# Kernel optimization log

Hardware: AMD Instinct MI355X
Metric: run time of the kernel (lower is better)

The kernel has to match this reference:

```python
import jax, jax.numpy as jnp
import numpy as np

BATCH, SEQ, IN, HID = 128, 512, 128, 1024

def setup_inputs() -> dict:
    key = jax.random.key(0)
    ks = jax.random.split(key, 7)
    s = 0.02  # small init so tanh/sigmoid stay in useful range
    return {
        "x": jax.random.normal(ks[0], (BATCH, SEQ, IN), dtype=jnp.float32),
        "W0": jax.random.normal(ks[1], (IN + HID, 3 * HID), dtype=jnp.float32) * s,
        "b0": jnp.zeros((3 * HID,), dtype=jnp.float32),
        "W1": jax.random.normal(ks[2], (HID + HID, 3 * HID), dtype=jnp.float32) * s,
        "b1": jnp.zeros((3 * HID,), dtype=jnp.float32),
        "Wfc": jax.random.normal(ks[3], (HID, 1), dtype=jnp.float32) * s,
        "bfc": jnp.zeros((1,), dtype=jnp.float32),
    }

def reference(x, W0, b0, W1, b1, Wfc, bfc):
    # Faithful to the torch module: note reset_gate/combined_reset are computed
    # but NEVER used for new_gate in the original -- new_gate = tanh(gates chunk 3)
    # from the [input, h_prev] projection. We reproduce that exact math.
    batch = x.shape[0]
    Ws, bs = (W0, W1), (b0, b1)
    h0 = tuple(jnp.zeros((batch, HID), dtype=x.dtype) for _ in range(2))

    def step(hs, x_t):
        inp = x_t
        new_hs = []
        for W, b, h in zip(Ws, bs, hs):
            gates = jnp.concatenate([inp, h], axis=1) @ W + b  # (B, 3H)
            z, _r, n = jnp.split(gates, 3, axis=1)
            z = jax.nn.sigmoid(z)
            n = jnp.tanh(n)
            h = (1.0 - z) * n + z * h
            new_hs.append(h)
            inp = h
        return tuple(new_hs), inp  # inp == last layer h_next

    x_t = jnp.transpose(x, (1, 0, 2))  # (S, B, IN)
    _, outs = jax.lax.scan(step, h0, x_t)  # outs: (S, B, H)
    # predictions[:, -1, :].squeeze(): only the final timestep matters
    pred_last = outs[-1] @ Wfc + bfc  # (B, 1)
    return jnp.squeeze(pred_last, axis=-1)  # (B,)
```

## Files before the change

### kernel.cpp

```cpp
#include <hip/hip_runtime.h>
#include <hip/hip_bf16.h>
#include <stdint.h>


#define SEQLEN 512
#define INDIM  128

typedef short bhalf8 __attribute__((ext_vector_type(8)));
typedef float f32x4  __attribute__((ext_vector_type(4)));

#define WS_H0B 4096
#define WS_H1B (WS_H0B + 2*262144)
#define WS_H1F (WS_H1B + 2*262144)
#define WS_END (WS_H1F + 524288)
#define LDS_BYTES 163840

__device__ __forceinline__ unsigned int bfbits(float f) {
  __hip_bfloat16 h = __float2bfloat16(f);
  unsigned short u; __builtin_memcpy(&u, &h, 2);
  return (unsigned int)u;
}

template<int N> __device__ __forceinline__ void waitvm() {
  asm volatile("s_waitcnt vmcnt(%0)" :: "n"(N));
}

#define GLOADA(dst, p)  asm volatile("global_load_dwordx4 %0, %1, off sc0 sc1" : "=v"(dst) : "v"((unsigned long long)(p)))
#define STORE_BF16(p, u) asm volatile("global_store_short %0, %1, off sc0 sc1" :: "v"((unsigned long long)(p)), "v"(u))
#define STORE_F32(p, f)  asm volatile("global_store_dword %0, %1, off sc0 sc1" :: "v"((unsigned long long)(p)), "v"(f))

#define ATIE(sI) asm volatile("" : "+v"(af[sI][0]), "+v"(af[sI][1]), "+v"(af[sI][2]), "+v"(af[sI][3]))

#define MFMA4(ntI, bx, sI) \
  acc[0][ntI] = __builtin_amdgcn_mfma_f32_16x16x32_bf16(af[sI][0], bx, acc[0][ntI], 0,0,0); \
  acc[1][ntI] = __builtin_amdgcn_mfma_f32_16x16x32_bf16(af[sI][1], bx, acc[1][ntI], 0,0,0); \
  acc[2][ntI] = __builtin_amdgcn_mfma_f32_16x16x32_bf16(af[sI][2], bx, acc[2][ntI], 0,0,0); \
  acc[3][ntI] = __builtin_amdgcn_mfma_f32_16x16x32_bf16(af[sI][3], bx, acc[3][ntI], 0,0,0);

#define MFMA4X(ntI, bx) \
  acc[0][ntI] = __builtin_amdgcn_mfma_f32_16x16x32_bf16(ax[0], bx, acc[0][ntI], 0,0,0); \
  acc[1][ntI] = __builtin_amdgcn_mfma_f32_16x16x32_bf16(ax[1], bx, acc[1][ntI], 0,0,0); \
  acc[2][ntI] = __builtin_amdgcn_mfma_f32_16x16x32_bf16(ax[2], bx, acc[2][ntI], 0,0,0); \
  acc[3][ntI] = __builtin_amdgcn_mfma_f32_16x16x32_bf16(ax[3], bx, acc[3][ntI], 0,0,0);

#define LDSB0(ntI, kb) (*(const bhalf8*)(smem + ((ntI)*16 + l15)*2304 + ((kb) ^ swz)))
#define LDSB1(ntI, kb) (*(const bhalf8*)(smem + ((ntI)*16 + l15)*4096 + ((kb) ^ swz)))

#define L0H(i) { \
  waitvm<((i) <= 4 ? 12 : 4*(7-(i)))>(); \
  ATIE((i)&3); \
  { const int kb = 256 + ks*512 + (i)*64 + l4*16; \
    bhalf8 bv0 = LDSB0(0, kb); bhalf8 bv1 = LDSB0(1, kb); \
    bhalf8 bv2 = LDSB0(2, kb); bhalf8 bv3 = LDSB0(3, kb); \
    MFMA4(0, bv0, (i)&3); MFMA4(1, bv1, (i)&3); \
    MFMA4(2, bv2, (i)&3); MFMA4(3, bv3, (i)&3); } \
  if ((i) + 4 < 8) { \
    GLOADA(af[(i)&3][0], abase0 + ((i)+4)*32); \
    GLOADA(af[(i)&3][1], abase1 + ((i)+4)*32); \
    GLOADA(af[(i)&3][2], abase2 + ((i)+4)*32); \
    GLOADA(af[(i)&3][3], abase3 + ((i)+4)*32); } \
}

#define L1H(i) { \
  waitvm<((i) <= 12 ? 12 : 4*(15-(i)))>(); \
  ATIE((i)&3); \
  { const int kb = ks*1024 + (i)*64 + l4*16; \
    bhalf8 bv0 = LDSB1(0, kb); bhalf8 bv1 = LDSB1(1, kb); \
    MFMA4(0, bv0, (i)&3); MFMA4(1, bv1, (i)&3); } \
  if ((i) + 4 < 16) { \
    GLOADA(af[(i)&3][0], abase0 + ((i)+4)*32); \
    GLOADA(af[(i)&3][1], abase1 + ((i)+4)*32); \
    GLOADA(af[(i)&3][2], abase2 + ((i)+4)*32); \
    GLOADA(af[(i)&3][3], abase3 + ((i)+4)*32); } \
}

__global__ __launch_bounds__(256, 1) void gru_persist(
    const float* __restrict__ x,  const float* __restrict__ W0,
    const float* __restrict__ b0, const float* __restrict__ W1,
    const float* __restrict__ b1, char* __restrict__ ws)
{
  extern __shared__ char smem[];
  const int tid  = threadIdx.x;
  const int lane = tid & 63;
  const int ks   = tid >> 6;
  const int l4   = lane >> 4;
  const int l15  = lane & 15;
  const int swz  = (l15 & 7) << 4;
  const int wg   = blockIdx.x;
  const bool isL0 = wg < 64;

  unsigned short* h0b = (unsigned short*)(ws + WS_H0B);
  unsigned short* h1b = (unsigned short*)(ws + WS_H1B);
  float*          h1f = (float*)(ws + WS_H1F);
  unsigned int*   bar = (unsigned int*)ws;

  int g, blk;
  if (isL0) { g = wg & 1; blk = wg >> 1; }
  else      { int idx = wg - 64; g = idx & 1; blk = idx >> 1; }

  if (isL0) {
    const int n   = lane;
    const int col = (n < 32) ? (blk*32 + n) : (2048 + blk*32 + (n - 32));
    for (int it = 0; it < 288; ++it) {
      const int k = ks*288 + it;
      unsigned int u = bfbits(W0[(size_t)k*3072 + col]);
      *(unsigned short*)(smem + n*2304 + ((2*k) ^ ((n & 7) << 4))) = (unsigned short)u;
    }
  } else {
    const int n   = lane & 31;
    const int col = (n < 16) ? (blk*16 + n) : (2048 + blk*16 + (n - 16));
    for (int it = 0; it < 256; ++it) {
      const int k = ks*512 + it*2 + (lane >> 5);
      unsigned int u = bfbits(W1[(size_t)k*3072 + col]);
      *(unsigned short*)(smem + n*4096 + ((2*k) ^ ((n & 7) << 4))) = (unsigned short)u;
    }
  }
  __syncthreads();

  float biasv[4] = {0.f, 0.f, 0.f, 0.f};
  if (isL0) {
    biasv[0] = b0[blk*32 + l15];
    biasv[1] = b0[blk*32 + 16 + l15];
    biasv[2] = b0[2048 + blk*32 + l15];
    biasv[3] = b0[2048 + blk*32 + 16 + l15];
  } else {
    biasv[0] = b1[blk*16 + l15];
    biasv[1] = b1[2048 + blk*16 + l15];
  }

  float hp[2][4] = {{0.f,0.f,0.f,0.f},{0.f,0.f,0.f,0.f}};

  for (int p = 0; p <= SEQLEN; ++p) {
    if (isL0) {
      if (p < SEQLEN) {
        const int t = p;
        const unsigned short* h0in  = h0b + (size_t)((t+1)&1)*131072;
        unsigned short*       h0out = h0b + (size_t)(t&1)*131072;

        f32x4 acc[4][4];
        #pragma unroll
        for (int mt = 0; mt < 4; ++mt)
          #pragma unroll
          for (int nt = 0; nt < 4; ++nt)
            #pragma unroll
            for (int r = 0; r < 4; ++r)
              acc[mt][nt][r] = (ks == 0) ? biasv[nt] : 0.0f;

        {
          bhalf8 ax[4];
          #pragma unroll
          for (int mt = 0; mt < 4; ++mt) {
            const int b = g*64 + mt*16 + l15;
            const float* xp = x + ((size_t)b*SEQLEN + t)*INDIM + ks*32 + l4*8;
            f32x4 lo = *(const f32x4*)xp;
            f32x4 hi = *(const f32x4*)(xp + 4);
            #pragma unroll
            for (int e = 0; e < 4; ++e) {
              ax[mt][e]   = (short)bfbits(lo[e]);
              ax[mt][4+e] = (short)bfbits(hi[e]);
            }
          }
          const int kb = ks*64 + l4*16;
          bhalf8 bv0 = LDSB0(0, kb); bhalf8 bv1 = LDSB0(1, kb);
          bhalf8 bv2 = LDSB0(2, kb); bhalf8 bv3 = LDSB0(3, kb);
          MFMA4X(0, bv0); MFMA4X(1, bv1); MFMA4X(2, bv2); MFMA4X(3, bv3);
        }

        const int bb = g*64 + l15;
        const unsigned short* abase0 = h0in + (size_t)(bb +  0)*1024 + ks*256 + l4*8;
        const unsigned short* abase1 = h0in + (size_t)(bb + 16)*1024 + ks*256 + l4*8;
        const unsigned short* abase2 = h0in + (size_t)(bb + 32)*1024 + ks*256 + l4*8;
        const unsigned short* abase3 = h0in + (size_t)(bb + 48)*1024 + ks*256 + l4*8;
        bhalf8 af[4][4];
        GLOADA(af[0][0], abase0 +  0); GLOADA(af[0][1], abase1 +  0);
        GLOADA(af[0][2], abase2 +  0); GLOADA(af[0][3], abase3 +  0);
        GLOADA(af[1][0], abase0 + 32); GLOADA(af[1][1], abase1 + 32);
        GLOADA(af[1][2], abase2 + 32); GLOADA(af[1][3], abase3 + 32);
        GLOADA(af[2][0], abase0 + 64); GLOADA(af[2][1], abase1 + 64);
        GLOADA(af[2][2], abase2 + 64); GLOADA(af[2][3], abase3 + 64);
        GLOADA(af[3][0], abase0 + 96); GLOADA(af[3][1], abase1 + 96);
        GLOADA(af[3][2], abase2 + 96); GLOADA(af[3][3], abase3 + 96);
        L0H(0) L0H(1) L0H(2) L0H(3) L0H(4) L0H(5) L0H(6) L0H(7)

        float* st = (float*)(smem + 147456);
        f32x4 gacc[4];
        #pragma unroll
        for (int q = 0; q < 4; ++q) {
          __syncthreads();
          #pragma unroll
          for (int nt = 0; nt < 4; ++nt)
            #pragma unroll
            for (int r = 0; r < 4; ++r)
              st[ks*1024 + nt*256 + (l4*4+r)*16 + l15] = acc[q][nt][r];
          __syncthreads();
          if (ks == q) {
            #pragma unroll
            for (int nt = 0; nt < 4; ++nt)
              #pragma unroll
              for (int r = 0; r < 4; ++r)
                gacc[nt][r] = st[       nt*256 + (l4*4+r)*16 + l15]
                            + st[1024 + nt*256 + (l4*4+r)*16 + l15]
                            + st[2048 + nt*256 + (l4*4+r)*16 + l15]
                            + st[3072 + nt*256 + (l4*4+r)*16 + l15];
          }
        }

        #pragma unroll
        for (int pi = 0; pi < 2; ++pi)
          #pragma unroll
          for (int r = 0; r < 4; ++r) {
            const float z  = 1.0f/(1.0f + __expf(-gacc[pi][r]));
            const float e2 = __expf(2.0f*gacc[pi+2][r]);
            const float n  = (e2 - 1.0f)/(e2 + 1.0f);
            const float hn = n + z*(hp[pi][r] - n);
            hp[pi][r] = hn;
            const int j = blk*32 + pi*16 + l15;
            const int b = g*64 + ks*16 + l4*4 + r;
            STORE_BF16(h0out + (size_t)b*1024 + j, bfbits(hn));
          }
      }
    } else {
      if (p > 0) {
        const int t = p - 1;
        const unsigned short* h0in  = h0b + (size_t)(t&1)*131072;
        const unsigned short* h1in  = h1b + (size_t)((t+1)&1)*131072;
        unsigned short*       h1out = h1b + (size_t)(t&1)*131072;

        f32x4 acc[4][2];
        #pragma unroll
        for (int mt = 0; mt < 4; ++mt)
          #pragma unroll
          for (int nt = 0; nt < 2; ++nt)
            #pragma unroll
            for (int r = 0; r < 4; ++r)
              acc[mt][nt][r] = (ks == 0) ? biasv[nt] : 0.0f;

        const unsigned short* asrc = (ks < 2) ? h0in : h1in;
        const int bb = g*64 + l15;
        const unsigned short* abase0 = asrc + (size_t)(bb +  0)*1024 + (ks&1)*512 + l4*8;
        const unsigned short* abase1 = asrc + (size_t)(bb + 16)*1024 + (ks&1)*512 + l4*8;
        const unsigned short* abase2 = asrc + (size_t)(bb + 32)*1024 + (ks&1)*512 + l4*8;
        const unsigned short* abase3 = asrc + (size_t)(bb + 48)*1024 + (ks&1)*512 + l4*8;
        bhalf8 af[4][4];
        GLOADA(af[0][0], abase0 +  0); GLOADA(af[0][1], abase1 +  0);
        GLOADA(af[0][2], abase2 +  0); GLOADA(af[0][3], abase3 +  0);
        GLOADA(af[1][0], abase0 + 32); GLOADA(af[1][1], abase1 + 32);
        GLOADA(af[1][2], abase2 + 32); GLOADA(af[1][3], abase3 + 32);
        GLOADA(af[2][0], abase0 + 64); GLOADA(af[2][1], abase1 + 64);
        GLOADA(af[2][2], abase2 + 64); GLOADA(af[2][3], abase3 + 64);
        GLOADA(af[3][0], abase0 + 96); GLOADA(af[3][1], abase1 + 96);
        GLOADA(af[3][2], abase2 + 96); GLOADA(af[3][3], abase3 + 96);
        L1H(0)  L1H(1)  L1H(2)  L1H(3)  L1H(4)  L1H(5)  L1H(6)  L1H(7)
        L1H(8)  L1H(9)  L1H(10) L1H(11) L1H(12) L1H(13) L1H(14) L1H(15)

        float* st = (float*)(smem + 131072);
        f32x4 gacc[2];
        #pragma unroll
        for (int q = 0; q < 4; ++q) {
          __syncthreads();
          #pragma unroll
          for (int nt = 0; nt < 2; ++nt)
            #pragma unroll
            for (int r = 0; r < 4; ++r)
              st[ks*512 + nt*256 + (l4*4+r)*16 + l15] = acc[q][nt][r];
          __syncthreads();
          if (ks == q) {
            #pragma unroll
            for (int nt = 0; nt < 2; ++nt)
              #pragma unroll
              for (int r = 0; r < 4; ++r)
                gacc[nt][r] = st[       nt*256 + (l4*4+r)*16 + l15]
                            + st[ 512 + nt*256 + (l4*4+r)*16 + l15]
                            + st[1024 + nt*256 + (l4*4+r)*16 + l15]
                            + st[1536 + nt*256 + (l4*4+r)*16 + l15];
          }
        }

        #pragma unroll
        for (int r = 0; r < 4; ++r) {
          const float z  = 1.0f/(1.0f + __expf(-gacc[0][r]));
          const float e2 = __expf(2.0f*gacc[1][r]);
          const float n  = (e2 - 1.0f)/(e2 + 1.0f);
          const float hn = n + z*(hp[0][r] - n);
          hp[0][r] = hn;
          const int j = blk*16 + l15;
          const int b = g*64 + ks*16 + l4*4 + r;
          STORE_BF16(h1out + (size_t)b*1024 + j, bfbits(hn));
          STORE_F32(h1f + (size_t)b*1024 + j, hn);
        }
      }
    }

    asm volatile("s_waitcnt vmcnt(0) lgkmcnt(0)" ::: "memory");
    __syncthreads();
    if (tid == 0) {
      __hip_atomic_fetch_add(&bar[(wg & 7)*32], 1u, __ATOMIC_RELAXED, __HIP_MEMORY_SCOPE_AGENT);
      const unsigned int target = 24u * (unsigned int)(p + 1);
      for (;;) {
        unsigned int mn = 0xffffffffu;
        #pragma unroll
        for (int c = 0; c < 8; ++c) {
          unsigned int v = __hip_atomic_load(&bar[c*32], __ATOMIC_RELAXED, __HIP_MEMORY_SCOPE_AGENT);
          mn = (v < mn) ? v : mn;
        }
        if (mn >= target) break;
        __builtin_amdgcn_s_sleep(1);
      }
    }
    __syncthreads();
  }
}

__global__ void gru_pred(const char* __restrict__ ws, const float* __restrict__ Wfc,
                         const float* __restrict__ bfc, float* __restrict__ out)
{
  const int b = blockIdx.x;
  const int l = threadIdx.x;
  const float* h = (const float*)(ws + WS_H1F) + (size_t)b*1024;
  float s = 0.0f;
  for (int k = l; k < 1024; k += 64) s += h[k] * Wfc[k];
  #pragma unroll
  for (int off = 32; off > 0; off >>= 1) s += __shfl_down(s, off);
  if (l == 0) out[b] = s + bfc[0];
}

extern "C" void kernel_launch(void* const* d_in, const int* in_sizes, int n_in,
                              void* d_out, int out_size, void* d_ws, size_t ws_size,
                              hipStream_t stream)
{
  (void)in_sizes; (void)n_in; (void)out_size; (void)ws_size;
  const float* x   = (const float*)d_in[0];
  const float* W0  = (const float*)d_in[1];
  const float* b0  = (const float*)d_in[2];
  const float* W1  = (const float*)d_in[3];
  const float* b1  = (const float*)d_in[4];
  const float* Wfc = (const float*)d_in[5];
  const float* bfc = (const float*)d_in[6];
  char* ws = (char*)d_ws;

  hipFuncSetAttribute(reinterpret_cast<const void*>(gru_persist),
                      hipFuncAttributeMaxDynamicSharedMemorySize, LDS_BYTES);
  hipMemsetAsync(ws, 0, WS_END, stream);
  hipLaunchKernelGGL(gru_persist, dim3(192), dim3(256), LDS_BYTES, stream,
                     x, W0, b0, W1, b1, ws);
  hipLaunchKernelGGL(gru_pred, dim3(128), dim3(64), 0, stream,
                     ws, Wfc, bfc, (float*)d_out);
}
```

Baseline: 5.835 ms.

## Replace global grid barrier with per-row-block dataflow flags and full-K waves

Replaces the per-timestep grid-wide atomic barrier with fine-grained per-row-block, per-column-group progress flags, so each wave waits only on the producers it actually reads. Each wave now covers the full K dimension for its own batch rows, which removes the cross-wave LDS split-K reduction and its __syncthreads. Hidden-state buffers are quadruple-buffered so layer 0 can run up to three steps ahead of layer 1. The layer-1 fp32 state is written only at the last step. The cost is more global loads per wave and many flag polls, and correctness now depends on the release fence and flag ordering.

New measurement: 13.78 ms. 136% more time.

```diff
diff --git a/kernel.cpp b/kernel.cpp
--- a/kernel.cpp
+++ b/kernel.cpp
@@ -4,310 +4,265 @@
 
 
 #define SEQLEN 512
-#define INDIM  128
 
 typedef short bhalf8 __attribute__((ext_vector_type(8)));
 typedef float f32x4  __attribute__((ext_vector_type(4)));
 
-#define WS_H0B 4096
-#define WS_H1B (WS_H0B + 2*262144)
-#define WS_H1F (WS_H1B + 2*262144)
-#define WS_END (WS_H1F + 524288)
-#define LDS_BYTES 163840
+#define OFF_F0   0
+#define OFF_F1   2048
+#define OFF_H0   8192
+#define OFF_H1   (OFF_H0 + 4*262144)
+#define OFF_H1F  (OFF_H1 + 4*262144)
+#define WS_END   (OFF_H1F + 524288)
+#define LDS_BYTES 131072
 
 __device__ __forceinline__ unsigned int bfbits(float f) {
   __hip_bfloat16 h = __float2bfloat16(f);
   unsigned short u; __builtin_memcpy(&u, &h, 2);
   return (unsigned int)u;
 }
-
 template<int N> __device__ __forceinline__ void waitvm() {
   asm volatile("s_waitcnt vmcnt(%0)" :: "n"(N));
 }
-
-#define GLOADA(dst, p)  asm volatile("global_load_dwordx4 %0, %1, off sc0 sc1" : "=v"(dst) : "v"((unsigned long long)(p)))
-#define STORE_BF16(p, u) asm volatile("global_store_short %0, %1, off sc0 sc1" :: "v"((unsigned long long)(p)), "v"(u))
-#define STORE_F32(p, f)  asm volatile("global_store_dword %0, %1, off sc0 sc1" :: "v"((unsigned long long)(p)), "v"(f))
-
-#define ATIE(sI) asm volatile("" : "+v"(af[sI][0]), "+v"(af[sI][1]), "+v"(af[sI][2]), "+v"(af[sI][3]))
-
-#define MFMA4(ntI, bx, sI) \
-  acc[0][ntI] = __builtin_amdgcn_mfma_f32_16x16x32_bf16(af[sI][0], bx, acc[0][ntI], 0,0,0); \
-  acc[1][ntI] = __builtin_amdgcn_mfma_f32_16x16x32_bf16(af[sI][1], bx, acc[1][ntI], 0,0,0); \
-  acc[2][ntI] = __builtin_amdgcn_mfma_f32_16x16x32_bf16(af[sI][2], bx, acc[2][ntI], 0,0,0); \
-  acc[3][ntI] = __builtin_amdgcn_mfma_f32_16x16x32_bf16(af[sI][3], bx, acc[3][ntI], 0,0,0);
-
-#define MFMA4X(ntI, bx) \
-  acc[0][ntI] = __builtin_amdgcn_mfma_f32_16x16x32_bf16(ax[0], bx, acc[0][ntI], 0,0,0); \
-  acc[1][ntI] = __builtin_amdgcn_mfma_f32_16x16x32_bf16(ax[1], bx, acc[1][ntI], 0,0,0); \
-  acc[2][ntI] = __builtin_amdgcn_mfma_f32_16x16x32_bf16(ax[2], bx, acc[2][ntI], 0,0,0); \
-  acc[3][ntI] = __builtin_amdgcn_mfma_f32_16x16x32_bf16(ax[3], bx, acc[3][ntI], 0,0,0);
-
-#define LDSB0(ntI, kb) (*(const bhalf8*)(smem + ((ntI)*16 + l15)*2304 + ((kb) ^ swz)))
-#define LDSB1(ntI, kb) (*(const bhalf8*)(smem + ((ntI)*16 + l15)*4096 + ((kb) ^ swz)))
-
-#define L0H(i) { \
-  waitvm<((i) <= 4 ? 12 : 4*(7-(i)))>(); \
-  ATIE((i)&3); \
-  { const int kb = 256 + ks*512 + (i)*64 + l4*16; \
-    bhalf8 bv0 = LDSB0(0, kb); bhalf8 bv1 = LDSB0(1, kb); \
-    bhalf8 bv2 = LDSB0(2, kb); bhalf8 bv3 = LDSB0(3, kb); \
-    MFMA4(0, bv0, (i)&3); MFMA4(1, bv1, (i)&3); \
-    MFMA4(2, bv2, (i)&3); MFMA4(3, bv3, (i)&3); } \
-  if ((i) + 4 < 8) { \
-    GLOADA(af[(i)&3][0], abase0 + ((i)+4)*32); \
-    GLOADA(af[(i)&3][1], abase1 + ((i)+4)*32); \
-    GLOADA(af[(i)&3][2], abase2 + ((i)+4)*32); \
-    GLOADA(af[(i)&3][3], abase3 + ((i)+4)*32); } \
-}
-
-#define L1H(i) { \
-  waitvm<((i) <= 12 ? 12 : 4*(15-(i)))>(); \
-  ATIE((i)&3); \
-  { const int kb = ks*1024 + (i)*64 + l4*16; \
-    bhalf8 bv0 = LDSB1(0, kb); bhalf8 bv1 = LDSB1(1, kb); \
-    MFMA4(0, bv0, (i)&3); MFMA4(1, bv1, (i)&3); } \
-  if ((i) + 4 < 16) { \
-    GLOADA(af[(i)&3][0], abase0 + ((i)+4)*32); \
-    GLOADA(af[(i)&3][1], abase1 + ((i)+4)*32); \
-    GLOADA(af[(i)&3][2], abase2 + ((i)+4)*32); \
-    GLOADA(af[(i)&3][3], abase3 + ((i)+4)*32); } \
-}
-
-__global__ __launch_bounds__(256, 1) void gru_persist(
+#define GLOADA(dst, p)  asm volatile("global_load_dwordx4 %0, %1, off sc0 sc1" : "=v"(dst) : "v"((unsigned long long)(p)) : "memory")
+#define STORE_BF16(p,u) asm volatile("global_store_short %0, %1, off sc0 sc1" :: "v"((unsigned long long)(p)), "v"(u) : "memory")
+#define STORE_F32(p,f)  asm volatile("global_store_dword %0, %1, off sc0 sc1" :: "v"((unsigned long long)(p)), "v"(f) : "memory")
+#define RELEASE_FENCE() __builtin_amdgcn_fence(__ATOMIC_RELEASE, "agent")
+
+#define MFMA(a,b,c) __builtin_amdgcn_mfma_f32_16x16x32_bf16((a),(b),(c),0,0,0)
+
+#define L0I(i) { \
+  waitvm<((i) < 28 ? 6 : 2*(31-(i)))>(); \
+  asm volatile("" : "+v"(af[(i)&3][0]), "+v"(af[(i)&3][1])); \
+  { const int kb = 256 + (i)*64 + l4*16; \
+    bhalf8 bvz = *(const bhalf8*)(smem + l15*2304 + (kb ^ swz)); \
+    bhalf8 bvn = *(const bhalf8*)(smem + (16+l15)*2304 + (kb ^ swz)); \
+    acc[0][0] = MFMA(af[(i)&3][0], bvz, acc[0][0]); \
+    acc[0][1] = MFMA(af[(i)&3][0], bvn, acc[0][1]); \
+    acc[1][0] = MFMA(af[(i)&3][1], bvz, acc[1][0]); \
+    acc[1][1] = MFMA(af[(i)&3][1], bvn, acc[1][1]); } \
+  if ((i)+4 < 32) { GLOADA(af[(i)&3][0], ab0 + ((i)+4)*32); \
+                    GLOADA(af[(i)&3][1], ab1 + ((i)+4)*32); } \
+}
+
+#define L1I(i, KOFF, abx) { \
+  waitvm<((i) < 24 ? 7 : (31-(i)))>(); \
+  asm volatile("" : "+v"(af[(i)&7])); \
+  { const int kb = (KOFF) + (i)*64 + l4*16; \
+    bhalf8 bvz = *(const bhalf8*)(smem + l15*4096 + (kb ^ swz)); \
+    bhalf8 bvn = *(const bhalf8*)(smem + (16+l15)*4096 + (kb ^ swz)); \
+    accz = MFMA(af[(i)&7], bvz, accz); \
+    accn = MFMA(af[(i)&7], bvn, accn); } \
+  if ((i)+8 < 32) { GLOADA(af[(i)&7], (abx) + ((i)+8)*32); } \
+}
+
+#define L1HALF(KOFF, abx) \
+  L1I(0,KOFF,abx)  L1I(1,KOFF,abx)  L1I(2,KOFF,abx)  L1I(3,KOFF,abx)  \
+  L1I(4,KOFF,abx)  L1I(5,KOFF,abx)  L1I(6,KOFF,abx)  L1I(7,KOFF,abx)  \
+  L1I(8,KOFF,abx)  L1I(9,KOFF,abx)  L1I(10,KOFF,abx) L1I(11,KOFF,abx) \
+  L1I(12,KOFF,abx) L1I(13,KOFF,abx) L1I(14,KOFF,abx) L1I(15,KOFF,abx) \
+  L1I(16,KOFF,abx) L1I(17,KOFF,abx) L1I(18,KOFF,abx) L1I(19,KOFF,abx) \
+  L1I(20,KOFF,abx) L1I(21,KOFF,abx) L1I(22,KOFF,abx) L1I(23,KOFF,abx) \
+  L1I(24,KOFF,abx) L1I(25,KOFF,abx) L1I(26,KOFF,abx) L1I(27,KOFF,abx) \
+  L1I(28,KOFF,abx) L1I(29,KOFF,abx) L1I(30,KOFF,abx) L1I(31,KOFF,abx)
+
+__global__ __launch_bounds__(256,1) void gru_persist(
     const float* __restrict__ x,  const float* __restrict__ W0,
     const float* __restrict__ b0, const float* __restrict__ W1,
     const float* __restrict__ b1, char* __restrict__ ws)
 {
   extern __shared__ char smem[];
-  const int tid  = threadIdx.x;
-  const int lane = tid & 63;
-  const int ks   = tid >> 6;
-  const int l4   = lane >> 4;
-  const int l15  = lane & 15;
-  const int swz  = (l15 & 7) << 4;
-  const int wg   = blockIdx.x;
+  const int tid = threadIdx.x, lane = tid & 63, wv = tid >> 6;
+  const int l4 = lane >> 4, l15 = lane & 15;
+  const int swz = (l15 & 7) << 4;
+  const int wg = blockIdx.x;
   const bool isL0 = wg < 64;
 
-  unsigned short* h0b = (unsigned short*)(ws + WS_H0B);
-  unsigned short* h1b = (unsigned short*)(ws + WS_H1B);
-  float*          h1f = (float*)(ws + WS_H1F);
-  unsigned int*   bar = (unsigned int*)ws;
-
-  int g, blk;
-  if (isL0) { g = wg & 1; blk = wg >> 1; }
-  else      { int idx = wg - 64; g = idx & 1; blk = idx >> 1; }
-
-  if (isL0) {
-    const int n   = lane;
-    const int col = (n < 32) ? (blk*32 + n) : (2048 + blk*32 + (n - 32));
-    for (int it = 0; it < 288; ++it) {
-      const int k = ks*288 + it;
-      unsigned int u = bfbits(W0[(size_t)k*3072 + col]);
-      *(unsigned short*)(smem + n*2304 + ((2*k) ^ ((n & 7) << 4))) = (unsigned short)u;
-    }
-  } else {
-    const int n   = lane & 31;
-    const int col = (n < 16) ? (blk*16 + n) : (2048 + blk*16 + (n - 16));
-    for (int it = 0; it < 256; ++it) {
-      const int k = ks*512 + it*2 + (lane >> 5);
-      unsigned int u = bfbits(W1[(size_t)k*3072 + col]);
-      *(unsigned short*)(smem + n*4096 + ((2*k) ^ ((n & 7) << 4))) = (unsigned short)u;
+  int* flags0 = (int*)(ws + OFF_F0);
+  int* flags1 = (int*)(ws + OFF_F1);
+  unsigned short* h0b = (unsigned short*)(ws + OFF_H0);
+  unsigned short* h1b = (unsigned short*)(ws + OFF_H1);
+  float*          h1f = (float*)(ws + OFF_H1F);
+
+  int cg, g = 0;
+  if (isL0) cg = wg;
+  else { cg = (wg - 64) >> 1; g = (wg - 64) & 1; }
+
+  {
+    const int n = tid & 31, kg = tid >> 5;
+    const int col = (n < 16) ? cg*16 + n : 2048 + cg*16 + (n - 16);
+    if (isL0) {
+      for (int it = 0; it < 144; ++it) {
+        const int k = kg*144 + it;
+        *(unsigned short*)(smem + n*2304 + ((2*k) ^ ((n&7)<<4))) =
+            (unsigned short)bfbits(W0[(size_t)k*3072 + col]);
+      }
+    } else {
+      for (int it = 0; it < 256; ++it) {
+        const int k = kg*256 + it;
+        *(unsigned short*)(smem + n*4096 + ((2*k) ^ ((n&7)<<4))) =
+            (unsigned short)bfbits(W1[(size_t)k*3072 + col]);
+      }
     }
   }
   __syncthreads();
 
-  float biasv[4] = {0.f, 0.f, 0.f, 0.f};
+  float bz, bn;
+  if (isL0) { bz = b0[cg*16 + l15]; bn = b0[2048 + cg*16 + l15]; }
+  else      { bz = b1[cg*16 + l15]; bn = b1[2048 + cg*16 + l15]; }
+
   if (isL0) {
-    biasv[0] = b0[blk*32 + l15];
-    biasv[1] = b0[blk*32 + 16 + l15];
-    biasv[2] = b0[2048 + blk*32 + l15];
-    biasv[3] = b0[2048 + blk*32 + 16 + l15];
-  } else {
-    biasv[0] = b1[blk*16 + l15];
-    biasv[1] = b1[2048 + blk*16 + l15];
-  }
-
-  float hp[2][4] = {{0.f,0.f,0.f,0.f},{0.f,0.f,0.f,0.f}};
-
-  for (int p = 0; p <= SEQLEN; ++p) {
-    if (isL0) {
-      if (p < SEQLEN) {
-        const int t = p;
-        const unsigned short* h0in  = h0b + (size_t)((t+1)&1)*131072;
-        unsigned short*       h0out = h0b + (size_t)(t&1)*131072;
-
-        f32x4 acc[4][4];
+    const int rb0 = 2*wv, rb1 = 2*wv + 1;
+    float hp[2][4] = {{0.f,0.f,0.f,0.f},{0.f,0.f,0.f,0.f}};
+    const int* f0a = flags0 + rb0*64 + lane;
+    const int* f0b = flags0 + rb1*64 + lane;
+    const int* f1a = flags1 + rb0*64 + lane;
+    const int* f1b = flags1 + rb1*64 + lane;
+
+    #pragma unroll 1
+    for (int t = 0; t < SEQLEN; ++t) {
+      f32x4 acc[2][2];
+      #pragma unroll
+      for (int mt = 0; mt < 2; ++mt)
         #pragma unroll
-        for (int mt = 0; mt < 4; ++mt)
+        for (int r = 0; r < 4; ++r) { acc[mt][0][r] = bz; acc[mt][1][r] = bn; }
+
+      #pragma unroll
+      for (int mt = 0; mt < 2; ++mt) {
+        const int b = wv*32 + mt*16 + l15;
+        const float* xp = x + ((size_t)b*SEQLEN + t)*128 + l4*8;
+        #pragma unroll
+        for (int kk = 0; kk < 4; ++kk) {
+          f32x4 lo = *(const f32x4*)(xp + kk*32);
+          f32x4 hi = *(const f32x4*)(xp + kk*32 + 4);
+          bhalf8 ax;
           #pragma unroll
-          for (int nt = 0; nt < 4; ++nt)
-            #pragma unroll
-            for (int r = 0; r < 4; ++r)
-              acc[mt][nt][r] = (ks == 0) ? biasv[nt] : 0.0f;
-
-        {
-          bhalf8 ax[4];
-          #pragma unroll
-          for (int mt = 0; mt < 4; ++mt) {
-            const int b = g*64 + mt*16 + l15;
-            const float* xp = x + ((size_t)b*SEQLEN + t)*INDIM + ks*32 + l4*8;
-            f32x4 lo = *(const f32x4*)xp;
-            f32x4 hi = *(const f32x4*)(xp + 4);
-            #pragma unroll
-            for (int e = 0; e < 4; ++e) {
-              ax[mt][e]   = (short)bfbits(lo[e]);
-              ax[mt][4+e] = (short)bfbits(hi[e]);
-            }
+          for (int e = 0; e < 4; ++e) {
+            ax[e]   = (short)bfbits(lo[e]);
+            ax[4+e] = (short)bfbits(hi[e]);
           }
-          const int kb = ks*64 + l4*16;
-          bhalf8 bv0 = LDSB0(0, kb); bhalf8 bv1 = LDSB0(1, kb);
-          bhalf8 bv2 = LDSB0(2, kb); bhalf8 bv3 = LDSB0(3, kb);
-          MFMA4X(0, bv0); MFMA4X(1, bv1); MFMA4X(2, bv2); MFMA4X(3, bv3);
+          const int kb = kk*64 + l4*16;
+          bhalf8 bvz = *(const bhalf8*)(smem + l15*2304 + (kb ^ swz));
+          bhalf8 bvn = *(const bhalf8*)(smem + (16+l15)*2304 + (kb ^ swz));
+          acc[mt][0] = MFMA(ax, bvz, acc[mt][0]);
+          acc[mt][1] = MFMA(ax, bvn, acc[mt][1]);
         }
-
-        const int bb = g*64 + l15;
-        const unsigned short* abase0 = h0in + (size_t)(bb +  0)*1024 + ks*256 + l4*8;
-        const unsigned short* abase1 = h0in + (size_t)(bb + 16)*1024 + ks*256 + l4*8;
-        const unsigned short* abase2 = h0in + (size_t)(bb + 32)*1024 + ks*256 + l4*8;
-        const unsigned short* abase3 = h0in + (size_t)(bb + 48)*1024 + ks*256 + l4*8;
-        bhalf8 af[4][4];
-        GLOADA(af[0][0], abase0 +  0); GLOADA(af[0][1], abase1 +  0);
-        GLOADA(af[0][2], abase2 +  0); GLOADA(af[0][3], abase3 +  0);
-        GLOADA(af[1][0], abase0 + 32); GLOADA(af[1][1], abase1 + 32);
-        GLOADA(af[1][2], abase2 + 32); GLOADA(af[1][3], abase3 + 32);
-        GLOADA(af[2][0], abase0 + 64); GLOADA(af[2][1], abase1 + 64);
-        GLOADA(af[2][2], abase2 + 64); GLOADA(af[2][3], abase3 + 64);
-        GLOADA(af[3][0], abase0 + 96); GLOADA(af[3][1], abase1 + 96);
-        GLOADA(af[3][2], abase2 + 96); GLOADA(af[3][3], abase3 + 96);
-        L0H(0) L0H(1) L0H(2) L0H(3) L0H(4) L0H(5) L0H(6) L0H(7)
-
-        float* st = (float*)(smem + 147456);
-        f32x4 gacc[4];
+      }
+
+      {
+        const int tgt0 = t, tgt1 = t - 3;
+        for (;;) {
+          int a  = __hip_atomic_load(f0a, __ATOMIC_RELAXED, __HIP_MEMORY_SCOPE_AGENT);
+          int b2 = __hip_atomic_load(f0b, __ATOMIC_RELAXED, __HIP_MEMORY_SCOPE_AGENT);
+          int c  = __hip_atomic_load(f1a, __ATOMIC_RELAXED, __HIP_MEMORY_SCOPE_AGENT);
+          int d  = __hip_atomic_load(f1b, __ATOMIC_RELAXED, __HIP_MEMORY_SCOPE_AGENT);
+          if (__all((a >= tgt0) && (b2 >= tgt0) && (c >= tgt1) && (d >= tgt1))) break;
+          __builtin_amdgcn_s_sleep(1);
+        }
+      }
+
+      {
+        const unsigned short* src = h0b + (size_t)((t+3)&3)*131072;
+        const unsigned short* ab0 = src + (size_t)(wv*32 +      l15)*1024 + l4*8;
+        const unsigned short* ab1 = src + (size_t)(wv*32 + 16 + l15)*1024 + l4*8;
+        bhalf8 af[4][2];
+        GLOADA(af[0][0], ab0+ 0); GLOADA(af[0][1], ab1+ 0);
+        GLOADA(af[1][0], ab0+32); GLOADA(af[1][1], ab1+32);
+        GLOADA(af[2][0], ab0+64); GLOADA(af[2][1], ab1+64);
+        GLOADA(af[3][0], ab0+96); GLOADA(af[3][1], ab1+96);
+        L0I(0)  L0I(1)  L0I(2)  L0I(3)  L0I(4)  L0I(5)  L0I(6)  L0I(7)
+        L0I(8)  L0I(9)  L0I(10) L0I(11) L0I(12) L0I(13) L0I(14) L0I(15)
+        L0I(16) L0I(17) L0I(18) L0I(19) L0I(20) L0I(21) L0I(22) L0I(23)
+        L0I(24) L0I(25) L0I(26) L0I(27) L0I(28) L0I(29) L0I(30) L0I(31)
+      }
+
+      {
+        unsigned short* h0out = h0b + (size_t)(t&3)*131072;
         #pragma unroll
-        for (int q = 0; q < 4; ++q) {
-          __syncthreads();
-          #pragma unroll
-          for (int nt = 0; nt < 4; ++nt)
-            #pragma unroll
-            for (int r = 0; r < 4; ++r)
-              st[ks*1024 + nt*256 + (l4*4+r)*16 + l15] = acc[q][nt][r];
-          __syncthreads();
-          if (ks == q) {
-            #pragma unroll
-            for (int nt = 0; nt < 4; ++nt)
-              #pragma unroll
-              for (int r = 0; r < 4; ++r)
-                gacc[nt][r] = st[       nt*256 + (l4*4+r)*16 + l15]
-                            + st[1024 + nt*256 + (l4*4+r)*16 + l15]
-                            + st[2048 + nt*256 + (l4*4+r)*16 + l15]
-                            + st[3072 + nt*256 + (l4*4+r)*16 + l15];
-          }
-        }
-
-        #pragma unroll
-        for (int pi = 0; pi < 2; ++pi)
+        for (int mt = 0; mt < 2; ++mt)
           #pragma unroll
           for (int r = 0; r < 4; ++r) {
-            const float z  = 1.0f/(1.0f + __expf(-gacc[pi][r]));
-            const float e2 = __expf(2.0f*gacc[pi+2][r]);
+            const float z  = 1.0f/(1.0f + __expf(-acc[mt][0][r]));
+            const float e2 = __expf(2.0f*acc[mt][1][r]);
             const float n  = (e2 - 1.0f)/(e2 + 1.0f);
-            const float hn = n + z*(hp[pi][r] - n);
-            hp[pi][r] = hn;
-            const int j = blk*32 + pi*16 + l15;
-            const int b = g*64 + ks*16 + l4*4 + r;
-            STORE_BF16(h0out + (size_t)b*1024 + j, bfbits(hn));
+            const float hn = n + z*(hp[mt][r] - n);
+            hp[mt][r] = hn;
+            const int row = wv*32 + mt*16 + l4*4 + r;
+            STORE_BF16(h0out + (size_t)row*1024 + cg*16 + l15, bfbits(hn));
           }
-      }
-    } else {
-      if (p > 0) {
-        const int t = p - 1;
-        const unsigned short* h0in  = h0b + (size_t)(t&1)*131072;
-        const unsigned short* h1in  = h1b + (size_t)((t+1)&1)*131072;
-        unsigned short*       h1out = h1b + (size_t)(t&1)*131072;
-
-        f32x4 acc[4][2];
-        #pragma unroll
-        for (int mt = 0; mt < 4; ++mt)
-          #pragma unroll
-          for (int nt = 0; nt < 2; ++nt)
-            #pragma unroll
-            for (int r = 0; r < 4; ++r)
-              acc[mt][nt][r] = (ks == 0) ? biasv[nt] : 0.0f;
-
-        const unsigned short* asrc = (ks < 2) ? h0in : h1in;
-        const int bb = g*64 + l15;
-        const unsigned short* abase0 = asrc + (size_t)(bb +  0)*1024 + (ks&1)*512 + l4*8;
-        const unsigned short* abase1 = asrc + (size_t)(bb + 16)*1024 + (ks&1)*512 + l4*8;
-        const unsigned short* abase2 = asrc + (size_t)(bb + 32)*1024 + (ks&1)*512 + l4*8;
-        const unsigned short* abase3 = asrc + (size_t)(bb + 48)*1024 + (ks&1)*512 + l4*8;
-        bhalf8 af[4][4];
-        GLOADA(af[0][0], abase0 +  0); GLOADA(af[0][1], abase1 +  0);
-        GLOADA(af[0][2], abase2 +  0); GLOADA(af[0][3], abase3 +  0);
-        GLOADA(af[1][0], abase0 + 32); GLOADA(af[1][1], abase1 + 32);
-        GLOADA(af[1][2], abase2 + 32); GLOADA(af[1][3], abase3 + 32);
-        GLOADA(af[2][0], abase0 + 64); GLOADA(af[2][1], abase1 + 64);
-        GLOADA(af[2][2], abase2 + 64); GLOADA(af[2][3], abase3 + 64);
-        GLOADA(af[3][0], abase0 + 96); GLOADA(af[3][1], abase1 + 96);
-        GLOADA(af[3][2], abase2 + 96); GLOADA(af[3][3], abase3 + 96);
-        L1H(0)  L1H(1)  L1H(2)  L1H(3)  L1H(4)  L1H(5)  L1H(6)  L1H(7)
-        L1H(8)  L1H(9)  L1H(10) L1H(11) L1H(12) L1H(13) L1H(14) L1H(15)
-
-        float* st = (float*)(smem + 131072);
-        f32x4 gacc[2];
-        #pragma unroll
-        for (int q = 0; q < 4; ++q) {
-          __syncthreads();
-          #pragma unroll
-          for (int nt = 0; nt < 2; ++nt)
-            #pragma unroll
-            for (int r = 0; r < 4; ++r)
-              st[ks*512 + nt*256 + (l4*4+r)*16 + l15] = acc[q][nt][r];
-          __syncthreads();
-          if (ks == q) {
-            #pragma unroll
-            for (int nt = 0; nt < 2; ++nt)
-              #pragma unroll
-              for (int r = 0; r < 4; ++r)
-                gacc[nt][r] = st[       nt*256 + (l4*4+r)*16 + l15]
-                            + st[ 512 + nt*256 + (l4*4+r)*16 + l15]
-                            + st[1024 + nt*256 + (l4*4+r)*16 + l15]
-                            + st[1536 + nt*256 + (l4*4+r)*16 + l15];
-          }
+        RELEASE_FENCE();
+        if (lane == 0) {
+          __hip_atomic_store(flags0 + rb0*64 + cg, t+1, __ATOMIC_RELAXED, __HIP_MEMORY_SCOPE_AGENT);
+          __hip_atomic_store(flags0 + rb1*64 + cg, t+1, __ATOMIC_RELAXED, __HIP_MEMORY_SCOPE_AGENT);
         }
-
+      }
+    }
+  } else {
+    const int rb = g*4 + wv;
+    const int rowbase = g*64 + wv*16;
+    float hp[4] = {0.f,0.f,0.f,0.f};
+    const int* f1p = flags1 + rb*64 + lane;
+    const int* f0p = flags0 + rb*64 + lane;
+
+    #pragma unroll 1
+    for (int t = 0; t < SEQLEN; ++t) {
+      f32x4 accz, accn;
+      #pragma unroll
+      for (int r = 0; r < 4; ++r) { accz[r] = bz; accn[r] = bn; }
+
+      for (;;) {
+        int a = __hip_atomic_load(f1p, __ATOMIC_RELAXED, __HIP_MEMORY_SCOPE_AGENT);
+        if (__all(a >= t)) break;
+        __builtin_amdgcn_s_sleep(1);
+      }
+
+      {
+        const unsigned short* src1 = h1b + (size_t)((t+3)&3)*131072;
+        const unsigned short* ab = src1 + (size_t)(rowbase + l15)*1024 + l4*8;
+        bhalf8 af[8];
+        GLOADA(af[0], ab+  0); GLOADA(af[1], ab+ 32);
+        GLOADA(af[2], ab+ 64); GLOADA(af[3], ab+ 96);
+        GLOADA(af[4], ab+128); GLOADA(af[5], ab+160);
+        GLOADA(af[6], ab+192); GLOADA(af[7], ab+224);
+        L1HALF(2048, ab)
+      }
+
+      for (;;) {
+        int a = __hip_atomic_load(f0p, __ATOMIC_RELAXED, __HIP_MEMORY_SCOPE_AGENT);
+        if (__all(a >= t+1)) break;
+        __builtin_amdgcn_s_sleep(1);
+      }
+
+      {
+        const unsigned short* src0 = h0b + (size_t)(t&3)*131072;
+        const unsigned short* ab2 = src0 + (size_t)(rowbase + l15)*1024 + l4*8;
+        bhalf8 af[8];
+        GLOADA(af[0], ab2+  0); GLOADA(af[1], ab2+ 32);
+        GLOADA(af[2], ab2+ 64); GLOADA(af[3], ab2+ 96);
+        GLOADA(af[4], ab2+128); GLOADA(af[5], ab2+160);
+        GLOADA(af[6], ab2+192); GLOADA(af[7], ab2+224);
+        L1HALF(0, ab2)
+      }
+
+      {
+        unsigned short* h1out = h1b + (size_t)(t&3)*131072;
         #pragma unroll
         for (int r = 0; r < 4; ++r) {
-          const float z  = 1.0f/(1.0f + __expf(-gacc[0][r]));
-          const float e2 = __expf(2.0f*gacc[1][r]);
+          const float z  = 1.0f/(1.0f + __expf(-accz[r]));
+          const float e2 = __expf(2.0f*accn[r]);
           const float n  = (e2 - 1.0f)/(e2 + 1.0f);
-          const float hn = n + z*(hp[0][r] - n);
-          hp[0][r] = hn;
-          const int j = blk*16 + l15;
-          const int b = g*64 + ks*16 + l4*4 + r;
-          STORE_BF16(h1out + (size_t)b*1024 + j, bfbits(hn));
-          STORE_F32(h1f + (size_t)b*1024 + j, hn);
+          const float hn = n + z*(hp[r] - n);
+          hp[r] = hn;
+          const int row = rowbase + l4*4 + r;
+          STORE_BF16(h1out + (size_t)row*1024 + cg*16 + l15, bfbits(hn));
+          if (t == SEQLEN-1)
+            STORE_F32(h1f + (size_t)row*1024 + cg*16 + l15, hn);
         }
+        RELEASE_FENCE();
+        if (lane == 0)
+          __hip_atomic_store(flags1 + rb*64 + cg, t+1, __ATOMIC_RELAXED, __HIP_MEMORY_SCOPE_AGENT);
       }
     }
-
-    asm volatile("s_waitcnt vmcnt(0) lgkmcnt(0)" ::: "memory");
-    __syncthreads();
-    if (tid == 0) {
-      __hip_atomic_fetch_add(&bar[(wg & 7)*32], 1u, __ATOMIC_RELAXED, __HIP_MEMORY_SCOPE_AGENT);
-      const unsigned int target = 24u * (unsigned int)(p + 1);
-      for (;;) {
-        unsigned int mn = 0xffffffffu;
-        #pragma unroll
-        for (int c = 0; c < 8; ++c) {
-          unsigned int v = __hip_atomic_load(&bar[c*32], __ATOMIC_RELAXED, __HIP_MEMORY_SCOPE_AGENT);
-          mn = (v < mn) ? v : mn;
-        }
-        if (mn >= target) break;
-        __builtin_amdgcn_s_sleep(1);
-      }
-    }
-    __syncthreads();
   }
 }
 
@@ -316,7 +271,7 @@
 {
   const int b = blockIdx.x;
   const int l = threadIdx.x;
-  const float* h = (const float*)(ws + WS_H1F) + (size_t)b*1024;
+  const float* h = (const float*)(ws + OFF_H1F) + (size_t)b*1024;
   float s = 0.0f;
   for (int k = l; k < 1024; k += 64) s += h[k] * Wfc[k];
   #pragma unroll
```
